# Performance work log

Hardware: AMD Instinct MI355X
Metric: run time of the kernel (lower is better)

## Reference

```python
import jax, jax.numpy as jnp
import numpy as np

NEG_INF = -1e9  # stand-in for -float(config.inf)

def setup_inputs() -> dict:
    key = jax.random.key(0)
    ks = jax.random.split(key, 4)
    B, T, C, H = 8, 2048, 1024, 64
    x = jax.random.normal(ks[0], (B, T, C), dtype=jnp.float32)
    w_k = jax.random.normal(ks[1], (C, H), dtype=jnp.float32) * (C ** -0.5)
    w_q = jax.random.normal(ks[2], (C, H), dtype=jnp.float32) * (C ** -0.5)
    w_v = jax.random.normal(ks[3], (C, H), dtype=jnp.float32) * (C ** -0.5)
    return {"x": x, "w_k": w_k, "w_q": w_q, "w_v": w_v}

def reference(x, w_k, w_q, w_v):
    B, T, C = x.shape
    k = jnp.einsum('btc,ch->bth', x, w_k)  # [B,T,H]
    q = jnp.einsum('btc,ch->bth', x, w_q)
    v = jnp.einsum('btc,ch->bth', x, w_v)
    # NOTE: original scales by C**-0.5 with C = n_emb (not head_size)
    wei = jnp.einsum('bth,bsh->bts', q, k) * (C ** -0.5)  # [B,T,T]
    causal = jnp.tril(jnp.ones((T, T), dtype=bool))
    wei = jnp.where(causal, wei, NEG_INF)
    wei = jax.nn.softmax(wei, axis=-1)
    out = jnp.einsum('bts,bsh->bth', wei, v)  # [B,T,H]
    return out
```

## Files before the change

kernel.cpp:

```cpp
#include <hip/hip_runtime.h>
#include <hip/hip_bf16.h>

#define B_ 8
#define T_ 2048
#define C_ 1024
#define H_ 64

typedef __bf16 bf16x8 __attribute__((ext_vector_type(8)));
typedef float f32x4 __attribute__((ext_vector_type(4)));

__device__ __forceinline__ unsigned short f2bf(float f) {
    union { float f; unsigned u; } v; v.f = f;
    unsigned u = v.u;
    u += 0x7fffu + ((u >> 16) & 1u);
    return (unsigned short)(u >> 16);
}

#define GLOAD16(g, l) __builtin_amdgcn_global_load_lds( \
    (const __attribute__((address_space(1))) void*)(g), \
    (__attribute__((address_space(3))) void*)(l), 16, 0, 0)

#define MFMA16(a, b, c) __builtin_amdgcn_mfma_f32_16x16x32_bf16(a, b, c, 0, 0, 0)

__global__ __launch_bounds__(256) void wtrans_kernel(const float* __restrict__ wk,
                              const float* __restrict__ wq,
                              const float* __restrict__ wv,
                              unsigned short* __restrict__ wt) {
    __shared__ unsigned short ls[64][72];
    const int m = blockIdx.x >> 4, kt = blockIdx.x & 15;
    const float* w = (m == 0) ? wk : (m == 1) ? wq : wv;
    const int tid = threadIdx.x;
    #pragma unroll
    for (int it = 0; it < 4; ++it) {
        int k = it * 16 + (tid >> 4);
        int c = (tid & 15) * 4;
        float4 f = *(const float4*)(w + (size_t)(kt * 64 + k) * 64 + c);
        ls[c][k] = f2bf(f.x); ls[c + 1][k] = f2bf(f.y);
        ls[c + 2][k] = f2bf(f.z); ls[c + 3][k] = f2bf(f.w);
    }
    __syncthreads();
    const int c = tid >> 2, kc = (tid & 3) * 16;
    unsigned short* dst = wt + (size_t)(m * 64 + c) * 1024 + kt * 64 + kc;
    *(uint4*)dst = *(const uint4*)&ls[c][kc];
    *(uint4*)(dst + 8) = *(const uint4*)&ls[c][kc + 8];
}

__global__ __launch_bounds__(256) void qkv_kernel(const float* __restrict__ x,
        const unsigned short* __restrict__ wt,
        unsigned short* __restrict__ kh,
        unsigned short* __restrict__ qh,
        unsigned short* __restrict__ vt) {
    __shared__ __attribute__((aligned(16))) char smem[2][32768];
    const int tid = threadIdx.x;
    const int wid = tid >> 6, lane = tid & 63;
    const int lq = lane & 15, g = lane >> 4;
    const int rg = wid & 1, cg = wid >> 1;
    const int row0 = blockIdx.x * 32;
    const char* xg = (const char*)x;
    const char* wtg = (const char*)wt;

    f32x4 acc[6] = {};

    auto stage = [&](char* buf, int k0) {
        #pragma unroll
        for (int R = 0; R < 2; ++R) {
            int o = R * 4096 + tid * 16;
            int row = o >> 8, inrow = o & 255;
            int src = inrow ^ ((row & 15) << 4);
            GLOAD16(xg + ((size_t)(row0 + row) * 4096 + (size_t)k0 * 4 + src), buf + o);
        }
        #pragma unroll
        for (int R = 0; R < 6; ++R) {
            int o = R * 4096 + tid * 16;
            int row = o >> 7, inrow = o & 127;
            int src = inrow ^ ((row & 7) << 4);
            GLOAD16(wtg + ((size_t)row * 2048 + (size_t)k0 * 2 + src), buf + 8192 + o);
        }
    };

    stage(smem[0], 0);
    asm volatile("s_waitcnt vmcnt(0)" ::: "memory");
    __syncthreads();

    for (int t = 0; t < 16; ++t) {
        char* cur = smem[t & 1];
        if (t < 15) stage(smem[(t + 1) & 1], (t + 1) * 64);

        const char* xb = cur;
        const char* wb = cur + 8192;
        bf16x8 a[2];
        #pragma unroll
        for (int ks = 0; ks < 2; ++ks) {
            int row = rg * 16 + lq;
            int kb0 = ks * 128 + g * 32;
            float4 f0 = *(const float4*)(xb + row * 256 + (kb0 ^ ((row & 15) << 4)));
            float4 f1 = *(const float4*)(xb + row * 256 + ((kb0 + 16) ^ ((row & 15) << 4)));
            union { unsigned short u[8]; bf16x8 v; } u;
            u.u[0] = f2bf(f0.x); u.u[1] = f2bf(f0.y); u.u[2] = f2bf(f0.z); u.u[3] = f2bf(f0.w);
            u.u[4] = f2bf(f1.x); u.u[5] = f2bf(f1.y); u.u[6] = f2bf(f1.z); u.u[7] = f2bf(f1.w);
            a[ks] = u.v;
        }
        #pragma unroll
        for (int j = 0; j < 6; ++j) {
            int row = cg * 96 + j * 16 + lq;
            #pragma unroll
            for (int ks = 0; ks < 2; ++ks) {
                int kb = ks * 64 + g * 16;
                bf16x8 bfrag = *(const bf16x8*)(wb + row * 128 + (kb ^ ((row & 7) << 4)));
                acc[j] = MFMA16(a[ks], bfrag, acc[j]);
            }
        }
        asm volatile("s_waitcnt vmcnt(0)" ::: "memory");
        __syncthreads();
    }

    #pragma unroll
    for (int j = 0; j < 6; ++j) {
        int col = cg * 96 + j * 16 + lq;
        int m = col >> 6, h = col & 63;
        #pragma unroll
        for (int r = 0; r < 4; ++r) {
            int grow = row0 + rg * 16 + g * 4 + r;
            float val = acc[j][r];
            if (m == 0) {
                kh[(size_t)grow * H_ + h] = f2bf(val);
            } else if (m == 1) {
                qh[(size_t)grow * H_ + h] = f2bf(val * 0.03125f);
            } else {
                int bb = grow >> 11, tt = grow & (T_ - 1);
                vt[((size_t)bb * H_ + h) * T_ + tt] = f2bf(val);
            }
        }
    }
}

__global__ __launch_bounds__(256) void attn_kernel(const unsigned short* __restrict__ kh,
        const unsigned short* __restrict__ qh,
        const unsigned short* __restrict__ vt,
        float* __restrict__ out,
        float* __restrict__ po, float* __restrict__ pml, int split) {
    __shared__ __attribute__((aligned(16))) char kv[2][16384];
    __shared__ __attribute__((aligned(16))) char pl[4][2048];
    const int tid = threadIdx.x;
    const int wid = tid >> 6, lane = tid & 63;
    const int lq = lane & 15, g = lane >> 4;

    int b, qt, c, nch;
    if (split) {
        int qtc = blockIdx.x >> 3; b = blockIdx.x & 7;
        qt = 31 - (qtc >> 3); c = qtc & 7;
        nch = (qt + 4) >> 2;
        if (c >= nch) return;
    } else {
        b = blockIdx.x & 7; qt = 31 - (blockIdx.x >> 3); c = 0; nch = 1;
    }
    const int qw = qt * 64 + wid * 16;
    const int q_glob = qw + lq;
    const int s_end_blk = qt * 64 + 64;
    const int sbeg = c << 8;
    const int send = (split && sbeg + 256 < s_end_blk) ? sbeg + 256 : s_end_blk;
    const int nt = (send - sbeg) >> 6;

    const char* khb = (const char*)kh + (size_t)b * T_ * H_ * 2;
    const char* vtb = (const char*)vt + (size_t)b * H_ * T_ * 2;
    const unsigned short* qhb = qh + (size_t)b * T_ * H_;

    bf16x8 qf0 = *(const bf16x8*)(qhb + (qw + lq) * H_ + g * 8);
    bf16x8 qf1 = *(const bf16x8*)(qhb + (qw + lq) * H_ + 32 + g * 8);

    auto stage = [&](char* buf, int s0) {
        #pragma unroll
        for (int R = 0; R < 2; ++R) {
            int o = R * 4096 + wid * 1024;
            int ob = o + lane * 16;
            int row = ob >> 7, inrow = ob & 127;
            int src = inrow ^ ((row & 7) << 4);
            GLOAD16(khb + (size_t)(s0 + row) * 128 + src, buf + o);
        }
        #pragma unroll
        for (int R = 0; R < 2; ++R) {
            int o = R * 4096 + wid * 1024;
            int ob = o + lane * 16;
            int row = ob >> 7, inrow = ob & 127;
            int src = inrow ^ ((row & 7) << 4);
            GLOAD16(vtb + (size_t)row * 4096 + (size_t)s0 * 2 + src, buf + 8192 + o);
        }
    };

    float m_run = -1e30f, l_run = 0.f;
    f32x4 o_acc[4] = {};
    char* pbase = pl[wid];
    const int pswz = (lq & 7) << 4;

    stage(kv[0], sbeg);
    asm volatile("s_waitcnt vmcnt(0)" ::: "memory");
    __syncthreads();

    for (int t = 0; t < nt; ++t) {
        const int s0 = sbeg + t * 64;
        char* cur = kv[t & 1];
        if (t + 1 < nt) stage(kv[(t + 1) & 1], s0 + 64);
        const bool domask = (s0 + 64 == s_end_blk);

        f32x4 sa[4];
        __builtin_amdgcn_s_setprio(1);
        #pragma unroll
        for (int st = 0; st < 4; ++st) {
            int row = st * 16 + lq;
            int swz = (row & 7) << 4;
            f32x4 a = {};
            bf16x8 k0 = *(const bf16x8*)(cur + row * 128 + ((g * 16) ^ swz));
            bf16x8 k1 = *(const bf16x8*)(cur + row * 128 + ((64 + g * 16) ^ swz));
            a = MFMA16(k0, qf0, a);
            a = MFMA16(k1, qf1, a);
            sa[st] = a;
        }
        __builtin_amdgcn_s_setprio(0);

        float p[4][4];
        float smax = -1e30f;
        #pragma unroll
        for (int st = 0; st < 4; ++st)
            #pragma unroll
            for (int r = 0; r < 4; ++r) {
                float v = sa[st][r];
                if (domask) {
                    int sg = s0 + st * 16 + g * 4 + r;
                    v = (sg <= q_glob) ? v : -1e30f;
                }
                p[st][r] = v;
                smax = fmaxf(smax, v);
            }
        smax = fmaxf(smax, __shfl_xor(smax, 16));
        smax = fmaxf(smax, __shfl_xor(smax, 32));
        const float m_new = fmaxf(m_run, smax);
        const float alpha = __expf(m_run - m_new);
        float lsum = 0.f;
        #pragma unroll
        for (int st = 0; st < 4; ++st)
            #pragma unroll
            for (int r = 0; r < 4; ++r) {
                p[st][r] = __expf(p[st][r] - m_new);
                lsum += p[st][r];
            }
        lsum += __shfl_xor(lsum, 16);
        lsum += __shfl_xor(lsum, 32);
        l_run = l_run * alpha + lsum;
        m_run = m_new;
        #pragma unroll
        for (int hc = 0; hc < 4; ++hc) o_acc[hc] *= alpha;

        #pragma unroll
        for (int st = 0; st < 4; ++st) {
            union { unsigned short u[4]; uint2 d; } pk;
            pk.u[0] = f2bf(p[st][0]); pk.u[1] = f2bf(p[st][1]);
            pk.u[2] = f2bf(p[st][2]); pk.u[3] = f2bf(p[st][3]);
            *(uint2*)(pbase + lq * 128 + ((st * 32 + g * 8) ^ pswz)) = pk.d;
        }

        __builtin_amdgcn_s_setprio(1);
        #pragma unroll
        for (int hc = 0; hc < 4; ++hc) {
            int row = hc * 16 + lq;
            int swz = (row & 7) << 4;
            #pragma unroll
            for (int ss = 0; ss < 2; ++ss) {
                bf16x8 vf = *(const bf16x8*)(cur + 8192 + row * 128 + ((ss * 64 + g * 16) ^ swz));
                bf16x8 pb = *(const bf16x8*)(pbase + lq * 128 + ((ss * 64 + g * 16) ^ pswz));
                o_acc[hc] = MFMA16(vf, pb, o_acc[hc]);
            }
        }
        __builtin_amdgcn_s_setprio(0);

        asm volatile("s_waitcnt vmcnt(0)" ::: "memory");
        __syncthreads();
    }

    if (nch == 1) {
        const float inv_l = 1.0f / l_run;
        float* ob = out + ((size_t)b * T_ + qw + lq) * H_;
        #pragma unroll
        for (int hc = 0; hc < 4; ++hc)
            #pragma unroll
            for (int r = 0; r < 4; ++r)
                ob[hc * 16 + g * 4 + r] = o_acc[hc][r] * inv_l;
    } else {
        const int slot = (b * 32 + qt) * 8 + c;
        float* poS = po + (size_t)slot * 4096;
        const int row = wid * 16 + lq;
        #pragma unroll
        for (int hc = 0; hc < 4; ++hc)
            #pragma unroll
            for (int r = 0; r < 4; ++r)
                poS[(size_t)row * 64 + hc * 16 + g * 4 + r] = o_acc[hc][r];
        if (g == 0) {
            pml[slot * 64 + row] = m_run;
            pml[131072 + slot * 64 + row] = l_run;
        }
    }
}

__global__ __launch_bounds__(256) void combine_kernel(const float* __restrict__ po,
        const float* __restrict__ pml, float* __restrict__ out) {
    const int bq = blockIdx.x >> 4, seg = blockIdx.x & 15;
    const int b = bq / 28, qt = 4 + bq % 28;
    const int nch = (qt + 4) >> 2;
    const int r = seg * 4 + (threadIdx.x >> 6);
    const int h = threadIdx.x & 63;
    const int base_slot = (b * 32 + qt) * 8;

    float mv[9], lv[9], ov[9];
    float m = -1e30f;
    #pragma unroll 9
    for (int cc = 0; cc < 9; ++cc) {
        if (cc < nch) {
            mv[cc] = pml[(base_slot + cc) * 64 + r];
            lv[cc] = pml[131072 + (base_slot + cc) * 64 + r];
            ov[cc] = po[(size_t)(base_slot + cc) * 4096 + r * 64 + h];
            m = fmaxf(m, mv[cc]);
        }
    }
    float lsum = 0.f, osum = 0.f;
    #pragma unroll 9
    for (int cc = 0; cc < 9; ++cc) {
        if (cc < nch) {
            float w = __expf(mv[cc] - m);
            lsum += lv[cc] * w;
            osum += ov[cc] * w;
        }
    }
    out[((size_t)b * T_ + qt * 64 + r) * H_ + h] = osum / lsum;
}

extern "C" void kernel_launch(void* const* d_in, const int* in_sizes, int n_in,
                              void* d_out, int out_size, void* d_ws, size_t ws_size,
                              hipStream_t stream) {
    const float* x  = (const float*)d_in[0];
    const float* wk = (const float*)d_in[1];
    const float* wq = (const float*)d_in[2];
    const float* wv = (const float*)d_in[3];
    float* out = (float*)d_out;

    char* ws = (char*)d_ws;
    unsigned short* kh = (unsigned short*)(ws);
    unsigned short* qh = (unsigned short*)(ws + (size_t)2 * 1024 * 1024);
    unsigned short* vt = (unsigned short*)(ws + (size_t)4 * 1024 * 1024);
    unsigned short* wt = (unsigned short*)(ws + (size_t)6 * 1024 * 1024);
    float* po  = (float*)(ws + (size_t)8 * 1024 * 1024);
    float* pml = (float*)(ws + (size_t)40 * 1024 * 1024);

    const bool split = ws_size >= (size_t)42 * 1024 * 1024;

    wtrans_kernel<<<dim3(48), dim3(256), 0, stream>>>(wk, wq, wv, wt);
    qkv_kernel<<<dim3(512), dim3(256), 0, stream>>>(x, wt, kh, qh, vt);
    attn_kernel<<<dim3(split ? 2048 : 256), dim3(256), 0, stream>>>(kh, qh, vt, out, po, pml, split ? 1 : 0);
    if (split)
        combine_kernel<<<dim3(3584), dim3(256), 0, stream>>>(po, pml, out);
}
```

Before: 59.97 us.

## Use 32x32 MFMA with 128-row query tiles and compact split-K scheduling

The attention kernel now uses 32x32x16 bf16 MFMA with each wave owning 32 query rows, so a block covers 128 queries. This halves K/V staging per query and cuts the number of blocks. Chunks are enumerated compactly through a triangular prefix function, which removes early-exit blocks, and per-wave tiles lying fully above the diagonal are skipped. The combine kernel and workspace layout are updated to match. The costs are fewer blocks to spread across CUs, more registers per wave, and a loop to decode block indices.

```diff
diff --git a/kernel.cpp b/kernel.cpp
--- a/kernel.cpp
+++ b/kernel.cpp
@@ -8,6 +8,7 @@
 
 typedef __bf16 bf16x8 __attribute__((ext_vector_type(8)));
 typedef float f32x4 __attribute__((ext_vector_type(4)));
+typedef float f32x16 __attribute__((ext_vector_type(16)));
 
 __device__ __forceinline__ unsigned short f2bf(float f) {
     union { float f; unsigned u; } v; v.f = f;
@@ -15,12 +16,17 @@
     u += 0x7fffu + ((u >> 16) & 1u);
     return (unsigned short)(u >> 16);
 }
+__device__ __forceinline__ int cumq(int j) {
+    int h = j >> 1;
+    return j + h * (h - 1) + (j & 1) * h;
+}
 
 #define GLOAD16(g, l) __builtin_amdgcn_global_load_lds( \
     (const __attribute__((address_space(1))) void*)(g), \
     (__attribute__((address_space(3))) void*)(l), 16, 0, 0)
 
 #define MFMA16(a, b, c) __builtin_amdgcn_mfma_f32_16x16x32_bf16(a, b, c, 0, 0, 0)
+#define MFMA32(a, b, c) __builtin_amdgcn_mfma_f32_32x32x16_bf16(a, b, c, 0, 0, 0)
 
 __global__ __launch_bounds__(256) void wtrans_kernel(const float* __restrict__ wk,
                               const float* __restrict__ wq,
@@ -140,33 +146,37 @@
         float* __restrict__ out,
         float* __restrict__ po, float* __restrict__ pml, int split) {
     __shared__ __attribute__((aligned(16))) char kv[2][16384];
-    __shared__ __attribute__((aligned(16))) char pl[4][2048];
+    __shared__ __attribute__((aligned(16))) char pl[4][4096];
     const int tid = threadIdx.x;
     const int wid = tid >> 6, lane = tid & 63;
-    const int lq = lane & 15, g = lane >> 4;
+    const int l31 = lane & 31, hi = lane >> 5;
 
     int b, qt, c, nch;
     if (split) {
-        int qtc = blockIdx.x >> 3; b = blockIdx.x & 7;
-        qt = 31 - (qtc >> 3); c = qtc & 7;
-        nch = (qt + 4) >> 2;
-        if (c >= nch) return;
+        b = blockIdx.x & 7;
+        int r = 71 - (blockIdx.x >> 3);
+        qt = 0;
+        for (int j = 15; j >= 0; --j) { if (r >= cumq(j)) { qt = j; break; } }
+        c = r - cumq(qt);
+        nch = (qt >> 1) + 1;
     } else {
-        b = blockIdx.x & 7; qt = 31 - (blockIdx.x >> 3); c = 0; nch = 1;
-    }
-    const int qw = qt * 64 + wid * 16;
-    const int q_glob = qw + lq;
-    const int s_end_blk = qt * 64 + 64;
+        b = blockIdx.x & 7; qt = 15 - (blockIdx.x >> 3); c = 0; nch = 1;
+    }
+    const int qw = qt * 128 + wid * 32;
+    const int q_glob = qw + l31;
+    const int s_end_blk = qt * 128 + 128;
     const int sbeg = c << 8;
     const int send = (split && sbeg + 256 < s_end_blk) ? sbeg + 256 : s_end_blk;
     const int nt = (send - sbeg) >> 6;
 
-    const char* khb = (const char*)kh + (size_t)b * T_ * H_ * 2;
-    const char* vtb = (const char*)vt + (size_t)b * H_ * T_ * 2;
-    const unsigned short* qhb = qh + (size_t)b * T_ * H_;
-
-    bf16x8 qf0 = *(const bf16x8*)(qhb + (qw + lq) * H_ + g * 8);
-    bf16x8 qf1 = *(const bf16x8*)(qhb + (qw + lq) * H_ + 32 + g * 8);
+    const char* khb = (const char*)kh + ((size_t)b << 18);
+    const char* vtb = (const char*)vt + ((size_t)b << 18);
+    const unsigned short* qhb = qh + ((size_t)b << 17);
+
+    bf16x8 qf[4];
+    #pragma unroll
+    for (int f = 0; f < 4; ++f)
+        qf[f] = *(const bf16x8*)((const char*)(qhb + (size_t)(qw + l31) * H_) + f * 32 + hi * 16);
 
     auto stage = [&](char* buf, int s0) {
         #pragma unroll
@@ -188,9 +198,10 @@
     };
 
     float m_run = -1e30f, l_run = 0.f;
-    f32x4 o_acc[4] = {};
+    f32x16 o0 = {}, o1 = {};
     char* pbase = pl[wid];
-    const int pswz = (lq & 7) << 4;
+    const int pswz = (l31 & 7) << 4;
+    const int kswz = (l31 & 7) << 4;
 
     stage(kv[0], sbeg);
     asm volatile("s_waitcnt vmcnt(0)" ::: "memory");
@@ -200,77 +211,71 @@
         const int s0 = sbeg + t * 64;
         char* cur = kv[t & 1];
         if (t + 1 < nt) stage(kv[(t + 1) & 1], s0 + 64);
-        const bool domask = (s0 + 64 == s_end_blk);
-
-        f32x4 sa[4];
-        __builtin_amdgcn_s_setprio(1);
-        #pragma unroll
-        for (int st = 0; st < 4; ++st) {
-            int row = st * 16 + lq;
-            int swz = (row & 7) << 4;
-            f32x4 a = {};
-            bf16x8 k0 = *(const bf16x8*)(cur + row * 128 + ((g * 16) ^ swz));
-            bf16x8 k1 = *(const bf16x8*)(cur + row * 128 + ((64 + g * 16) ^ swz));
-            a = MFMA16(k0, qf0, a);
-            a = MFMA16(k1, qf1, a);
-            sa[st] = a;
-        }
-        __builtin_amdgcn_s_setprio(0);
-
-        float p[4][4];
-        float smax = -1e30f;
-        #pragma unroll
-        for (int st = 0; st < 4; ++st)
-            #pragma unroll
-            for (int r = 0; r < 4; ++r) {
-                float v = sa[st][r];
+        const bool active = (s0 < qw + 32);
+
+        if (active) {
+            const bool domask = (s0 + 64 > qw);
+            f32x16 sa0 = {}, sa1 = {};
+            __builtin_amdgcn_s_setprio(1);
+            #pragma unroll
+            for (int f = 0; f < 4; ++f) {
+                bf16x8 k0 = *(const bf16x8*)(cur + l31 * 128 + ((f * 32 + hi * 16) ^ kswz));
+                bf16x8 k1 = *(const bf16x8*)(cur + (32 + l31) * 128 + ((f * 32 + hi * 16) ^ kswz));
+                sa0 = MFMA32(k0, qf[f], sa0);
+                sa1 = MFMA32(k1, qf[f], sa1);
+            }
+            __builtin_amdgcn_s_setprio(0);
+
+            float p0[16], p1[16];
+            float smax = -1e30f;
+            #pragma unroll
+            for (int r = 0; r < 16; ++r) {
+                int srow = (r & 3) + 8 * (r >> 2) + 4 * hi;
+                float v0 = sa0[r], v1 = sa1[r];
                 if (domask) {
-                    int sg = s0 + st * 16 + g * 4 + r;
-                    v = (sg <= q_glob) ? v : -1e30f;
+                    if (s0 + srow > q_glob) v0 = -1e30f;
+                    if (s0 + 32 + srow > q_glob) v1 = -1e30f;
                 }
-                p[st][r] = v;
-                smax = fmaxf(smax, v);
-            }
-        smax = fmaxf(smax, __shfl_xor(smax, 16));
-        smax = fmaxf(smax, __shfl_xor(smax, 32));
-        const float m_new = fmaxf(m_run, smax);
-        const float alpha = __expf(m_run - m_new);
-        float lsum = 0.f;
-        #pragma unroll
-        for (int st = 0; st < 4; ++st)
-            #pragma unroll
-            for (int r = 0; r < 4; ++r) {
-                p[st][r] = __expf(p[st][r] - m_new);
-                lsum += p[st][r];
-            }
-        lsum += __shfl_xor(lsum, 16);
-        lsum += __shfl_xor(lsum, 32);
-        l_run = l_run * alpha + lsum;
-        m_run = m_new;
-        #pragma unroll
-        for (int hc = 0; hc < 4; ++hc) o_acc[hc] *= alpha;
-
-        #pragma unroll
-        for (int st = 0; st < 4; ++st) {
-            union { unsigned short u[4]; uint2 d; } pk;
-            pk.u[0] = f2bf(p[st][0]); pk.u[1] = f2bf(p[st][1]);
-            pk.u[2] = f2bf(p[st][2]); pk.u[3] = f2bf(p[st][3]);
-            *(uint2*)(pbase + lq * 128 + ((st * 32 + g * 8) ^ pswz)) = pk.d;
-        }
-
-        __builtin_amdgcn_s_setprio(1);
-        #pragma unroll
-        for (int hc = 0; hc < 4; ++hc) {
-            int row = hc * 16 + lq;
-            int swz = (row & 7) << 4;
-            #pragma unroll
-            for (int ss = 0; ss < 2; ++ss) {
-                bf16x8 vf = *(const bf16x8*)(cur + 8192 + row * 128 + ((ss * 64 + g * 16) ^ swz));
-                bf16x8 pb = *(const bf16x8*)(pbase + lq * 128 + ((ss * 64 + g * 16) ^ pswz));
-                o_acc[hc] = MFMA16(vf, pb, o_acc[hc]);
-            }
-        }
-        __builtin_amdgcn_s_setprio(0);
+                p0[r] = v0; p1[r] = v1;
+                smax = fmaxf(smax, fmaxf(v0, v1));
+            }
+            smax = fmaxf(smax, __shfl_xor(smax, 32));
+            const float m_new = fmaxf(m_run, smax);
+            const float alpha = __expf(m_run - m_new);
+            float lsum = 0.f;
+            #pragma unroll
+            for (int r = 0; r < 16; ++r) {
+                p0[r] = __expf(p0[r] - m_new);
+                p1[r] = __expf(p1[r] - m_new);
+                lsum += p0[r] + p1[r];
+            }
+            lsum += __shfl_xor(lsum, 32);
+            l_run = l_run * alpha + lsum;
+            m_run = m_new;
+            o0 *= alpha; o1 *= alpha;
+
+            #pragma unroll
+            for (int rq = 0; rq < 4; ++rq) {
+                uint2 d0, d1;
+                d0.x = (unsigned)f2bf(p0[rq * 4 + 0]) | ((unsigned)f2bf(p0[rq * 4 + 1]) << 16);
+                d0.y = (unsigned)f2bf(p0[rq * 4 + 2]) | ((unsigned)f2bf(p0[rq * 4 + 3]) << 16);
+                d1.x = (unsigned)f2bf(p1[rq * 4 + 0]) | ((unsigned)f2bf(p1[rq * 4 + 1]) << 16);
+                d1.y = (unsigned)f2bf(p1[rq * 4 + 2]) | ((unsigned)f2bf(p1[rq * 4 + 3]) << 16);
+                *(uint2*)(pbase + l31 * 128 + ((rq * 16 + hi * 8) ^ pswz)) = d0;
+                *(uint2*)(pbase + l31 * 128 + ((64 + rq * 16 + hi * 8) ^ pswz)) = d1;
+            }
+
+            __builtin_amdgcn_s_setprio(1);
+            #pragma unroll
+            for (int f = 0; f < 4; ++f) {
+                bf16x8 pb = *(const bf16x8*)(pbase + l31 * 128 + ((f * 32 + hi * 16) ^ pswz));
+                bf16x8 v0 = *(const bf16x8*)(cur + 8192 + l31 * 128 + ((f * 32 + hi * 16) ^ kswz));
+                bf16x8 v1 = *(const bf16x8*)(cur + 8192 + (32 + l31) * 128 + ((f * 32 + hi * 16) ^ kswz));
+                o0 = MFMA32(v0, pb, o0);
+                o1 = MFMA32(v1, pb, o1);
+            }
+            __builtin_amdgcn_s_setprio(0);
+        }
 
         asm volatile("s_waitcnt vmcnt(0)" ::: "memory");
         __syncthreads();
@@ -278,58 +283,68 @@
 
     if (nch == 1) {
         const float inv_l = 1.0f / l_run;
-        float* ob = out + ((size_t)b * T_ + qw + lq) * H_;
-        #pragma unroll
-        for (int hc = 0; hc < 4; ++hc)
-            #pragma unroll
-            for (int r = 0; r < 4; ++r)
-                ob[hc * 16 + g * 4 + r] = o_acc[hc][r] * inv_l;
+        float* ob = out + ((size_t)b * T_ + qw + l31) * H_;
+        #pragma unroll
+        for (int rq = 0; rq < 4; ++rq) {
+            float4 s0v, s1v;
+            s0v.x = o0[rq * 4 + 0] * inv_l; s0v.y = o0[rq * 4 + 1] * inv_l;
+            s0v.z = o0[rq * 4 + 2] * inv_l; s0v.w = o0[rq * 4 + 3] * inv_l;
+            s1v.x = o1[rq * 4 + 0] * inv_l; s1v.y = o1[rq * 4 + 1] * inv_l;
+            s1v.z = o1[rq * 4 + 2] * inv_l; s1v.w = o1[rq * 4 + 3] * inv_l;
+            *(float4*)(ob + rq * 8 + hi * 4) = s0v;
+            *(float4*)(ob + 32 + rq * 8 + hi * 4) = s1v;
+        }
     } else {
-        const int slot = (b * 32 + qt) * 8 + c;
-        float* poS = po + (size_t)slot * 4096;
-        const int row = wid * 16 + lq;
-        #pragma unroll
-        for (int hc = 0; hc < 4; ++hc)
-            #pragma unroll
-            for (int r = 0; r < 4; ++r)
-                poS[(size_t)row * 64 + hc * 16 + g * 4 + r] = o_acc[hc][r];
-        if (g == 0) {
-            pml[slot * 64 + row] = m_run;
-            pml[131072 + slot * 64 + row] = l_run;
+        const int slot = b * 72 + cumq(qt) + c;
+        float* poS = po + (size_t)slot * 8192 + (size_t)(wid * 32 + l31) * 64;
+        #pragma unroll
+        for (int rq = 0; rq < 4; ++rq) {
+            float4 s0v, s1v;
+            s0v.x = o0[rq * 4 + 0]; s0v.y = o0[rq * 4 + 1];
+            s0v.z = o0[rq * 4 + 2]; s0v.w = o0[rq * 4 + 3];
+            s1v.x = o1[rq * 4 + 0]; s1v.y = o1[rq * 4 + 1];
+            s1v.z = o1[rq * 4 + 2]; s1v.w = o1[rq * 4 + 3];
+            *(float4*)(poS + rq * 8 + hi * 4) = s0v;
+            *(float4*)(poS + 32 + rq * 8 + hi * 4) = s1v;
+        }
+        if (hi == 0) {
+            pml[slot * 128 + wid * 32 + l31] = m_run;
+            pml[73728 + slot * 128 + wid * 32 + l31] = l_run;
         }
     }
 }
 
 __global__ __launch_bounds__(256) void combine_kernel(const float* __restrict__ po,
         const float* __restrict__ pml, float* __restrict__ out) {
-    const int bq = blockIdx.x >> 4, seg = blockIdx.x & 15;
-    const int b = bq / 28, qt = 4 + bq % 28;
-    const int nch = (qt + 4) >> 2;
+    const int b = blockIdx.x / 448;
+    const int rem = blockIdx.x % 448;
+    const int qt = 2 + rem / 32, seg = rem % 32;
+    const int nch = (qt >> 1) + 1;
     const int r = seg * 4 + (threadIdx.x >> 6);
     const int h = threadIdx.x & 63;
-    const int base_slot = (b * 32 + qt) * 8;
-
-    float mv[9], lv[9], ov[9];
+    const int base_slot = b * 72 + cumq(qt);
+
+    float mv[8], lv[8], ov[8];
     float m = -1e30f;
-    #pragma unroll 9
-    for (int cc = 0; cc < 9; ++cc) {
+    #pragma unroll 8
+    for (int cc = 0; cc < 8; ++cc) {
         if (cc < nch) {
-            mv[cc] = pml[(base_slot + cc) * 64 + r];
-            lv[cc] = pml[131072 + (base_slot + cc) * 64 + r];
-            ov[cc] = po[(size_t)(base_slot + cc) * 4096 + r * 64 + h];
+            mv[cc] = pml[(base_slot + cc) * 128 + r];
+            lv[cc] = pml[73728 + (base_slot + cc) * 128 + r];
+            ov[cc] = po[(size_t)(base_slot + cc) * 8192 + r * 64 + h];
             m = fmaxf(m, mv[cc]);
         }
     }
     float lsum = 0.f, osum = 0.f;
-    #pragma unroll 9
-    for (int cc = 0; cc < 9; ++cc) {
+    #pragma unroll 8
+    for (int cc = 0; cc < 8; ++cc) {
         if (cc < nch) {
             float w = __expf(mv[cc] - m);
             lsum += lv[cc] * w;
             osum += ov[cc] * w;
         }
     }
-    out[((size_t)b * T_ + qt * 64 + r) * H_ + h] = osum / lsum;
+    out[((size_t)b * T_ + qt * 128 + r) * H_ + h] = osum / lsum;
 }
 
 extern "C" void kernel_launch(void* const* d_in, const int* in_sizes, int n_in,
@@ -347,13 +362,13 @@
     unsigned short* vt = (unsigned short*)(ws + (size_t)4 * 1024 * 1024);
     unsigned short* wt = (unsigned short*)(ws + (size_t)6 * 1024 * 1024);
     float* po  = (float*)(ws + (size_t)8 * 1024 * 1024);
-    float* pml = (float*)(ws + (size_t)40 * 1024 * 1024);
-
-    const bool split = ws_size >= (size_t)42 * 1024 * 1024;
+    float* pml = (float*)(ws + (size_t)28 * 1024 * 1024);
+
+    const bool split = ws_size >= (size_t)30 * 1024 * 1024;
 
     wtrans_kernel<<<dim3(48), dim3(256), 0, stream>>>(wk, wq, wv, wt);
     qkv_kernel<<<dim3(512), dim3(256), 0, stream>>>(x, wt, kh, qh, vt);
-    attn_kernel<<<dim3(split ? 2048 : 256), dim3(256), 0, stream>>>(kh, qh, vt, out, po, pml, split ? 1 : 0);
+    attn_kernel<<<dim3(split ? 576 : 128), dim3(256), 0, stream>>>(kh, qh, vt, out, po, pml, split ? 1 : 0);
     if (split)
         combine_kernel<<<dim3(3584), dim3(256), 0, stream>>>(po, pml, out);
 }
```

After: 63.67 us. +6.2%, slower.

## Fuse split-KV combine into attention kernel via last-block atomic counter

Applied to the files above, without the earlier changes.

Removes the separate combine kernel. Each split attention block writes its partial output and its max/sum stats, fences, then increments a per-(batch, query-tile) counter. The block that arrives last merges all chunks for its 64 rows. A memset that zeroes the counters is added before the launch. This saves one kernel launch and the work of a second grid, but the final merge now runs serially inside one block per tile, which can lengthen the tail.

```diff
diff --git a/kernel.cpp b/kernel.cpp
--- a/kernel.cpp
+++ b/kernel.cpp
@@ -138,9 +138,11 @@
         const unsigned short* __restrict__ qh,
         const unsigned short* __restrict__ vt,
         float* __restrict__ out,
-        float* __restrict__ po, float* __restrict__ pml, int split) {
+        float* __restrict__ po, float* __restrict__ pml,
+        int* __restrict__ cnt, int split) {
     __shared__ __attribute__((aligned(16))) char kv[2][16384];
     __shared__ __attribute__((aligned(16))) char pl[4][2048];
+    __shared__ int lastflag;
     const int tid = threadIdx.x;
     const int wid = tid >> 6, lane = tid & 63;
     const int lq = lane & 15, g = lane >> 4;
@@ -284,52 +286,59 @@
             #pragma unroll
             for (int r = 0; r < 4; ++r)
                 ob[hc * 16 + g * 4 + r] = o_acc[hc][r] * inv_l;
-    } else {
-        const int slot = (b * 32 + qt) * 8 + c;
-        float* poS = po + (size_t)slot * 4096;
-        const int row = wid * 16 + lq;
-        #pragma unroll
-        for (int hc = 0; hc < 4; ++hc)
-            #pragma unroll
-            for (int r = 0; r < 4; ++r)
-                poS[(size_t)row * 64 + hc * 16 + g * 4 + r] = o_acc[hc][r];
-        if (g == 0) {
-            pml[slot * 64 + row] = m_run;
-            pml[131072 + slot * 64 + row] = l_run;
-        }
-    }
-}
-
-__global__ __launch_bounds__(256) void combine_kernel(const float* __restrict__ po,
-        const float* __restrict__ pml, float* __restrict__ out) {
-    const int bq = blockIdx.x >> 4, seg = blockIdx.x & 15;
-    const int b = bq / 28, qt = 4 + bq % 28;
-    const int nch = (qt + 4) >> 2;
-    const int r = seg * 4 + (threadIdx.x >> 6);
-    const int h = threadIdx.x & 63;
+        return;
+    }
+
+    const int slot = (b * 32 + qt) * 8 + c;
+    float* poS = po + (size_t)slot * 4096;
+    const int prow = wid * 16 + lq;
+    #pragma unroll
+    for (int hc = 0; hc < 4; ++hc)
+        #pragma unroll
+        for (int r = 0; r < 4; ++r)
+            poS[(size_t)prow * 64 + hc * 16 + g * 4 + r] = o_acc[hc][r];
+    if (g == 0) {
+        pml[slot * 64 + prow] = m_run;
+        pml[131072 + slot * 64 + prow] = l_run;
+    }
+
+    __threadfence();
+    __syncthreads();
+    if (tid == 0) {
+        int prev = atomicAdd(&cnt[b * 32 + qt], 1);
+        lastflag = (prev == nch - 1) ? 1 : 0;
+    }
+    __syncthreads();
+    if (!lastflag) return;
+    __threadfence();
+
     const int base_slot = (b * 32 + qt) * 8;
-
-    float mv[9], lv[9], ov[9];
-    float m = -1e30f;
-    #pragma unroll 9
-    for (int cc = 0; cc < 9; ++cc) {
-        if (cc < nch) {
-            mv[cc] = pml[(base_slot + cc) * 64 + r];
-            lv[cc] = pml[131072 + (base_slot + cc) * 64 + r];
-            ov[cc] = po[(size_t)(base_slot + cc) * 4096 + r * 64 + h];
-            m = fmaxf(m, mv[cc]);
-        }
-    }
-    float lsum = 0.f, osum = 0.f;
-    #pragma unroll 9
-    for (int cc = 0; cc < 9; ++cc) {
-        if (cc < nch) {
-            float w = __expf(mv[cc] - m);
-            lsum += lv[cc] * w;
-            osum += ov[cc] * w;
-        }
-    }
-    out[((size_t)b * T_ + qt * 64 + r) * H_ + h] = osum / lsum;
+    const int h = tid & 63;
+    #pragma unroll 4
+    for (int rr = 0; rr < 16; ++rr) {
+        const int r = rr * 4 + (tid >> 6);
+        float mv[8], lv[8], ov[8];
+        float m = -1e30f;
+        #pragma unroll 8
+        for (int cc = 0; cc < 8; ++cc) {
+            if (cc < nch) {
+                mv[cc] = pml[(base_slot + cc) * 64 + r];
+                lv[cc] = pml[131072 + (base_slot + cc) * 64 + r];
+                ov[cc] = po[(size_t)(base_slot + cc) * 4096 + r * 64 + h];
+                m = fmaxf(m, mv[cc]);
+            }
+        }
+        float lsum = 0.f, osum = 0.f;
+        #pragma unroll 8
+        for (int cc = 0; cc < 8; ++cc) {
+            if (cc < nch) {
+                float w = __expf(mv[cc] - m);
+                lsum += lv[cc] * w;
+                osum += ov[cc] * w;
+            }
+        }
+        out[((size_t)b * T_ + qt * 64 + r) * H_ + h] = osum / lsum;
+    }
 }
 
 extern "C" void kernel_launch(void* const* d_in, const int* in_sizes, int n_in,
@@ -348,12 +357,16 @@
     unsigned short* wt = (unsigned short*)(ws + (size_t)6 * 1024 * 1024);
     float* po  = (float*)(ws + (size_t)8 * 1024 * 1024);
     float* pml = (float*)(ws + (size_t)40 * 1024 * 1024);
+    int*   cnt = (int*)(ws + (size_t)41 * 1024 * 1024);
 
     const bool split = ws_size >= (size_t)42 * 1024 * 1024;
 
     wtrans_kernel<<<dim3(48), dim3(256), 0, stream>>>(wk, wq, wv, wt);
     qkv_kernel<<<dim3(512), dim3(256), 0, stream>>>(x, wt, kh, qh, vt);
-    attn_kernel<<<dim3(split ? 2048 : 256), dim3(256), 0, stream>>>(kh, qh, vt, out, po, pml, split ? 1 : 0);
-    if (split)
-        combine_kernel<<<dim3(3584), dim3(256), 0, stream>>>(po, pml, out);
-}
+    if (split) {
+        hipMemsetAsync(cnt, 0, 256 * sizeof(int), stream);
+        attn_kernel<<<dim3(2048), dim3(256), 0, stream>>>(kh, qh, vt, out, po, pml, cnt, 1);
+    } else {
+        attn_kernel<<<dim3(256), dim3(256), 0, stream>>>(kh, qh, vt, out, po, pml, cnt, 0);
+    }
+}
```

After: 213.8 us. 257% more time.
